# Kernel optimization log

Hardware: AMD Instinct MI355X
Metric: run time of the kernel (lower is better)

## Reference

```python
import jax, jax.numpy as jnp
import numpy as np

K = 27  # num_neighs, hardcoded in module
EPS = 1e-5


def knn_idx(x, k):
    # x: (B, N, 3) -> (B, N, k) indices of k nearest neighbors (self included)
    xx = jnp.sum(x * x, axis=-1)                      # (B, N)
    inner = jnp.einsum('bnd,bmd->bnm', x, x)          # (B, N, N)
    d = 2.0 * inner - xx[:, :, None] - xx[:, None, :] # negative sq dist
    return jax.lax.top_k(d, k)[1]


def graph_feature(f, idx):
    # f: (B, N, C), idx: (B, N, k) -> (B, N, k, 2C) = [neigh - center, center]
    neigh = jax.vmap(lambda fb, ib: fb[ib])(f, idx)   # (B, N, k, C)
    center = jnp.broadcast_to(f[:, :, None, :], neigh.shape)
    return jnp.concatenate([neigh - center, center], axis=-1)


def bn_lrelu(y, g, b, axes):
    m = jnp.mean(y, axis=axes, keepdims=True)
    v = jnp.var(y, axis=axes, keepdims=True)
    y = (y - m) * jax.lax.rsqrt(v + EPS) * g + b
    return jnp.where(y >= 0, y, 0.2 * y)


def edge_conv(f, idx, W, g, b):
    # f: (B, N, C) -> (B, N, C_out); 1x1 conv over (B, 2C, N, k) + BN + LeakyReLU + max over k
    h = graph_feature(f, idx)                         # (B, N, k, 2C)
    y = jnp.einsum('bnkc,oc->bnko', h, W)             # (B, N, k, C_out)
    y = bn_lrelu(y, g, b, axes=(0, 1, 2))
    return jnp.max(y, axis=2)                         # (B, N, C_out)


def setup_inputs() -> dict:
    key = jax.random.key(0)
    ks = jax.random.split(key, 8)
    B, N, latent = 2, 2048, 256
    x = jax.random.normal(ks[0], (B, N, 3), dtype=jnp.float32)
    chans = [(6, 96), (192, 192), (384, 384), (768, 768)]
    inp = {'x': x}
    for i, (cin, cout) in enumerate(chans):
        inp[f'W{i}'] = jax.random.normal(ks[1 + i], (cout, cin), dtype=jnp.float32) * np.sqrt(2.0 / cin).astype(np.float32)
        inp[f'g{i}'] = jnp.ones((cout,), dtype=jnp.float32)
        inp[f'b{i}'] = jnp.zeros((cout,), dtype=jnp.float32)
    inp['W4'] = jax.random.normal(ks[5], (latent, 1440), dtype=jnp.float32) * np.sqrt(2.0 / 1440).astype(np.float32)
    inp['g4'] = jnp.ones((latent,), dtype=jnp.float32)
    inp['b4'] = jnp.zeros((latent,), dtype=jnp.float32)
    return inp


def reference(x, W0, g0, b0, W1, g1, b1, W2, g2, b2, W3, g3, b3, W4, g4, b4):
    # x: (B, N, 3)
    idx = knn_idx(x, K)                               # (B, N, K), fixed for all layers (only_true_neighs=True)
    outs = []
    f = x
    for (W, g, b) in ((W0, g0, b0), (W1, g1, b1), (W2, g2, b2), (W3, g3, b3)):
        f = edge_conv(f, idx, W, g, b)
        outs.append(f)
    h = jnp.concatenate(outs, axis=-1)                # (B, N, 1440)
    y = jnp.einsum('bnc,oc->bno', h, W4)              # (B, N, latent)
    feats = bn_lrelu(y, g4, b4, axes=(0, 1))          # features_per_point (B, N, latent)
    global_feat = jnp.max(feats, axis=1)              # (B, latent)
    return global_feat, feats
```

## Files before the change

kernel.cpp:

```cpp
#include <hip/hip_runtime.h>
#include <hip/hip_bf16.h>

#define BATCH 2
#define NPB   2048
#define NPTS  4096
#define KNB   27
#define FCATC 1440
#define CSTRIDE 1696
#define NSLOT 32
#define PBATCH 4

typedef __hip_bfloat16 bf16;
typedef __attribute__((ext_vector_type(8))) short short8;
typedef __attribute__((ext_vector_type(4))) float f32x4;

__device__ __forceinline__ float b2f(bf16 v) { return __bfloat162float(v); }

__device__ __forceinline__ void split_bf16(float v, bf16& h, bf16& l) {
    h = __float2bfloat16(v);
    l = __float2bfloat16(v - b2f(h));
}

__device__ __forceinline__ float ldin(const void* p, size_t i, int f32) {
    return f32 ? ((const float*)p)[i] : b2f(((const bf16*)p)[i]);
}

__global__ void k_detect(const void* __restrict__ x, int* __restrict__ flag) {
    __shared__ int s;
    if (threadIdx.x == 0) s = 0;
    __syncthreads();
    const bf16* xb = (const bf16*)x;
    int local = 0;
    for (int i = threadIdx.x; i < NPTS * 3; i += 256) {
        float v = b2f(xb[i]);
        if (!(fabsf(v) < 1e4f)) local = 1;
    }
    if (local) s = 1;
    __syncthreads();
    if (threadIdx.x == 0) flag[0] = s;
}

__global__ void k_convx(const void* __restrict__ x, const int* __restrict__ flag, float* __restrict__ xf) {
    int i = blockIdx.x * 256 + threadIdx.x;
    if (i >= NPTS * 3) return;
    xf[i] = ldin(x, i, flag[0]);
}

__global__ void k_zero(float* p, int n) {
    int i = blockIdx.x * 256 + threadIdx.x;
    if (i < n) p[i] = 0.f;
}

__global__ __launch_bounds__(256) void k_knn(const float* __restrict__ x, int* __restrict__ idx) {
    __shared__ uint hist4[4][260];
    __shared__ uint hist[256];
    __shared__ int  tix[NPB];
    __shared__ uint s_phigh;
    __shared__ int  s_rem, s_outcnt, s_tiecnt;

    int bn = blockIdx.x, b = bn >> 11, n = bn & (NPB - 1);
    int tid = threadIdx.x;
    int wv = tid >> 6;
    const float* xb = x + (size_t)b * NPB * 3;
    float cx = xb[n * 3 + 0], cy = xb[n * 3 + 1], cz = xb[n * 3 + 2];
    float cc = cx * cx + cy * cy + cz * cz;

    uint u[8];
    #pragma unroll
    for (int j = 0; j < 8; j++) {
        int m = j * 256 + tid;
        float mx = xb[m * 3 + 0], my = xb[m * 3 + 1], mz = xb[m * 3 + 2];
        float d = 2.f * (cx * mx + cy * my + cz * mz) - cc - (mx * mx + my * my + mz * mz);
        uint s = __float_as_uint(d);
        u[j] = (s & 0x80000000u) ? ~s : (s | 0x80000000u);
    }
    if (tid == 0) { s_phigh = 0; s_rem = KNB; s_outcnt = 0; s_tiecnt = 0; }

    for (int pass = 0; pass < 4; pass++) {
        int shift = 24 - pass * 8;
        hist[tid] = 0;
        for (int i = tid; i < 4 * 260; i += 256) ((uint*)hist4)[i] = 0;
        __syncthreads();
        uint phigh = s_phigh;
        #pragma unroll
        for (int j = 0; j < 8; j++) {
            bool in = (pass == 0) || ((u[j] >> (shift + 8)) == phigh);
            if (in) atomicAdd(&hist4[wv][(u[j] >> shift) & 0xFFu], 1u);
        }
        __syncthreads();
        hist[tid] = hist4[0][tid] + hist4[1][tid] + hist4[2][tid] + hist4[3][tid];
        __syncthreads();
        if (tid < 64) {
            int L = tid;
            uint c0 = hist[L * 4 + 0], c1 = hist[L * 4 + 1], c2 = hist[L * 4 + 2], c3 = hist[L * 4 + 3];
            uint s = c0 + c1 + c2 + c3;
            uint acc = s;
            #pragma unroll
            for (int off = 1; off < 64; off <<= 1) {
                uint t = __shfl_down(acc, off);
                if (L + off < 64) acc += t;
            }
            uint excl = acc - s;
            int rem = s_rem;
            if ((int)excl < rem && (int)acc >= rem) {
                uint cs[4] = { c0, c1, c2, c3 };
                uint cum = excl;
                int bsel = 0; uint hb = 0;
                #pragma unroll
                for (int q = 3; q >= 0; q--) {
                    if ((int)cum < rem && (int)(cum + cs[q]) >= rem && hb == 0u && bsel == 0) {
                        bsel = L * 4 + q; hb = cs[q]; cum += cs[q];
                    } else if (bsel == 0 && hb == 0u) {
                        cum += cs[q];
                    }
                }
                int strictlyAbove = (int)(cum - hb);
                s_rem = rem - strictlyAbove;
                s_phigh = (phigh << 8) | (uint)bsel;
            }
        }
        __syncthreads();
    }

    uint T = s_phigh;
    #pragma unroll
    for (int j = 0; j < 8; j++) {
        int m = j * 256 + tid;
        if (u[j] > T) {
            int p = atomicAdd(&s_outcnt, 1);
            idx[bn * KNB + p] = b * NPB + m;
        } else if (u[j] == T) {
            int p = atomicAdd(&s_tiecnt, 1);
            tix[p] = m;
        }
    }
    __syncthreads();
    int outcnt = s_outcnt, rem = s_rem, tiecnt = s_tiecnt;
    if (tiecnt == rem) {
        if (tid < rem) idx[bn * KNB + outcnt + tid] = b * NPB + tix[tid];
    } else if (tid == 0) {
        for (int t = 0; t < rem; t++) {
            int bi = 0;
            for (int q = 1; q < tiecnt; q++) if (tix[q] < tix[bi]) bi = q;
            idx[bn * KNB + outcnt + t] = b * NPB + tix[bi];
            tix[bi] = 0x7fffffff;
        }
    }
}

__global__ void k_l0(const float* __restrict__ xf, const void* __restrict__ W,
                     const int* __restrict__ flag, bf16* __restrict__ Ub, float* __restrict__ Vf) {
    int i = blockIdx.x * 256 + threadIdx.x;
    if (i >= NPTS * 192) return;
    int bn = i / 192, o = i % 192;
    int f32 = flag[0];
    float x0 = xf[bn * 3 + 0], x1 = xf[bn * 3 + 1], x2 = xf[bn * 3 + 2];
    if (o < 96) {
        float r = x0 * ldin(W, o * 6 + 0, f32) + x1 * ldin(W, o * 6 + 1, f32) + x2 * ldin(W, o * 6 + 2, f32);
        Ub[(size_t)bn * 96 + o] = __float2bfloat16(r);
    } else {
        int oo = o - 96;
        float w0 = ldin(W, oo * 6 + 3, f32) - ldin(W, oo * 6 + 0, f32);
        float w1 = ldin(W, oo * 6 + 4, f32) - ldin(W, oo * 6 + 1, f32);
        float w2 = ldin(W, oo * 6 + 5, f32) - ldin(W, oo * 6 + 2, f32);
        Vf[(size_t)bn * 96 + oo] = x0 * w0 + x1 * w1 + x2 * w2;
    }
}

__global__ void k_wtT(const void* __restrict__ W, const int* __restrict__ flag,
                      bf16* __restrict__ Wh, bf16* __restrict__ Wl, int Cin, int Co) {
    int o = blockIdx.x;
    int f32 = flag[0];
    for (int c = threadIdx.x; c < Cin; c += 256) {
        float w;
        if (o < Co) {
            w = ldin(W, (size_t)o * 2 * Cin + c, f32);
        } else {
            int oo = o - Co;
            w = ldin(W, (size_t)oo * 2 * Cin + Cin + c, f32) - ldin(W, (size_t)oo * 2 * Cin + c, f32);
        }
        bf16 h, l; split_bf16(w, h, l);
        Wh[(size_t)o * Cin + c] = h;
        Wl[(size_t)o * Cin + c] = l;
    }
}

__global__ void k_wtT4(const void* __restrict__ W4, const int* __restrict__ flag,
                       bf16* __restrict__ Wh, bf16* __restrict__ Wl) {
    int i = blockIdx.x * 256 + threadIdx.x;
    if (i >= 256 * FCATC) return;
    bf16 h, l; split_bf16(ldin(W4, i, flag[0]), h, l);
    Wh[i] = h; Wl[i] = l;
}

__global__ __launch_bounds__(256) void k_gemm_mfma(const bf16* __restrict__ Ah, const bf16* __restrict__ Al,
                                                   int lda, int aoff,
                                                   const bf16* __restrict__ Bh, const bf16* __restrict__ Bl,
                                                   int K, bf16* __restrict__ Cu, float* __restrict__ Cv,
                                                   int Cosplit, int ldc, int ksz, int zstride) {
    __shared__ bf16 Ash[64][40];
    __shared__ bf16 Asl[64][40];
    __shared__ bf16 Bsh[64][40];
    __shared__ bf16 Bsl[64][40];
    int tid = threadIdx.x;
    int wave = tid >> 6, lane = tid & 63;
    int wm = wave >> 1, wn = wave & 1;
    int quad = lane >> 4, l15 = lane & 15;
    int Lxy = blockIdx.y * gridDim.x + blockIdx.x;
    int stripe = Lxy & 7;
    int w = Lxy >> 3;
    int mb = stripe * 8 + (w & 7);
    int nb = w >> 3;
    int m0 = mb * 64, n0 = nb * 64;
    int kbase = blockIdx.z * ksz;
    float* Cz = Cv + (size_t)blockIdx.z * zstride;
    int lr = tid >> 2, lc = (tid & 3) * 8;

    f32x4 acc[2][2] = {};
    for (int k0 = kbase; k0 < kbase + ksz; k0 += 32) {
        size_t ao = (size_t)(m0 + lr) * lda + aoff + k0 + lc;
        size_t bo = (size_t)(n0 + lr) * K + k0 + lc;
        *(short8*)&Ash[lr][lc] = *(const short8*)&Ah[ao];
        *(short8*)&Asl[lr][lc] = *(const short8*)&Al[ao];
        *(short8*)&Bsh[lr][lc] = *(const short8*)&Bh[bo];
        *(short8*)&Bsl[lr][lc] = *(const short8*)&Bl[bo];
        __syncthreads();
        short8 ah0 = *(const short8*)&Ash[wm * 32 + l15][quad * 8];
        short8 ah1 = *(const short8*)&Ash[wm * 32 + 16 + l15][quad * 8];
        short8 al0 = *(const short8*)&Asl[wm * 32 + l15][quad * 8];
        short8 al1 = *(const short8*)&Asl[wm * 32 + 16 + l15][quad * 8];
        short8 bh0 = *(const short8*)&Bsh[wn * 32 + l15][quad * 8];
        short8 bh1 = *(const short8*)&Bsh[wn * 32 + 16 + l15][quad * 8];
        short8 bl0 = *(const short8*)&Bsl[wn * 32 + l15][quad * 8];
        short8 bl1 = *(const short8*)&Bsl[wn * 32 + 16 + l15][quad * 8];
        acc[0][0] = __builtin_amdgcn_mfma_f32_16x16x32_bf16(ah0, bl0, acc[0][0], 0, 0, 0);
        acc[0][0] = __builtin_amdgcn_mfma_f32_16x16x32_bf16(al0, bh0, acc[0][0], 0, 0, 0);
        acc[0][0] = __builtin_amdgcn_mfma_f32_16x16x32_bf16(ah0, bh0, acc[0][0], 0, 0, 0);
        acc[0][1] = __builtin_amdgcn_mfma_f32_16x16x32_bf16(ah0, bl1, acc[0][1], 0, 0, 0);
        acc[0][1] = __builtin_amdgcn_mfma_f32_16x16x32_bf16(al0, bh1, acc[0][1], 0, 0, 0);
        acc[0][1] = __builtin_amdgcn_mfma_f32_16x16x32_bf16(ah0, bh1, acc[0][1], 0, 0, 0);
        acc[1][0] = __builtin_amdgcn_mfma_f32_16x16x32_bf16(ah1, bl0, acc[1][0], 0, 0, 0);
        acc[1][0] = __builtin_amdgcn_mfma_f32_16x16x32_bf16(al1, bh0, acc[1][0], 0, 0, 0);
        acc[1][0] = __builtin_amdgcn_mfma_f32_16x16x32_bf16(ah1, bh0, acc[1][0], 0, 0, 0);
        acc[1][1] = __builtin_amdgcn_mfma_f32_16x16x32_bf16(ah1, bl1, acc[1][1], 0, 0, 0);
        acc[1][1] = __builtin_amdgcn_mfma_f32_16x16x32_bf16(al1, bh1, acc[1][1], 0, 0, 0);
        acc[1][1] = __builtin_amdgcn_mfma_f32_16x16x32_bf16(ah1, bh1, acc[1][1], 0, 0, 0);
        __syncthreads();
    }
    #pragma unroll
    for (int mt = 0; mt < 2; mt++) {
        #pragma unroll
        for (int nt = 0; nt < 2; nt++) {
            int col = n0 + wn * 32 + nt * 16 + l15;
            #pragma unroll
            for (int i = 0; i < 4; i++) {
                int row = m0 + wm * 32 + mt * 16 + quad * 4 + i;
                if (Cosplit > 0) {
                    if (col < Cosplit) Cu[(size_t)row * Cosplit + col] = __float2bfloat16(acc[mt][nt][i]);
                    else               Cv[(size_t)row * Cosplit + col - Cosplit] = acc[mt][nt][i];
                } else {
                    Cz[(size_t)row * ldc + col] = acc[mt][nt][i];
                }
            }
        }
    }
}

__global__ __launch_bounds__(256) void k_gather(const bf16* __restrict__ Ub, float* __restrict__ Vf,
                                                const int* __restrict__ idx,
                                                bf16* __restrict__ fch, bf16* __restrict__ fcl,
                                                float* __restrict__ ssum, float* __restrict__ ssq,
                                                int Co, int out_off) {
    __shared__ int srow[PBATCH * KNB];
    int tid = threadIdx.x;
    int L = blockIdx.y * gridDim.x + blockIdx.x;
    int batch = L & 1;
    int w = L >> 1;
    int pg = batch * 512 + (w & 511);
    int chunk = w >> 9;
    int p0 = pg * PBATCH;
    if (tid < PBATCH * KNB) srow[tid] = idx[p0 * KNB + tid] * Co;
    __syncthreads();
    int o = chunk * 256 + tid;
    if (o >= Co) return;
    int slot = pg & (NSLOT - 1);
    float s = 0.f, q = 0.f;
    #pragma unroll 1
    for (int p = 0; p < PBATCH; p++) {
        int bn = p0 + p;
        float v = Vf[(size_t)bn * Co + o];
        float ymax = -INFINITY, ymin = INFINITY;
        #pragma unroll
        for (int k = 0; k < KNB; k++) {
            float y = b2f(Ub[(size_t)srow[p * KNB + k] + o]) + v;
            ymax = fmaxf(ymax, y);
            ymin = fminf(ymin, y);
            s += y; q += y * y;
        }
        bf16 h, l; split_bf16(ymax, h, l);
        fch[(size_t)bn * FCATC + out_off + o] = h;
        fcl[(size_t)bn * FCATC + out_off + o] = l;
        Vf[(size_t)bn * Co + o] = ymin;
    }
    atomicAdd(&ssum[slot * CSTRIDE + o], s);
    atomicAdd(&ssq [slot * CSTRIDE + o], q);
}

__global__ void k_scaleshift(const float* __restrict__ ssum, const float* __restrict__ ssq,
                             const void* __restrict__ g, const void* __restrict__ bb,
                             const int* __restrict__ flag,
                             float* __restrict__ scale, float* __restrict__ shift, int Co, float invcnt) {
    int o = blockIdx.x * 256 + threadIdx.x;
    if (o >= Co) return;
    int f32 = flag[0];
    float s = 0.f, q = 0.f;
    for (int c = 0; c < NSLOT; c++) { s += ssum[c * CSTRIDE + o]; q += ssq[c * CSTRIDE + o]; }
    float mean = s * invcnt;
    float var = q * invcnt - mean * mean;
    float sc = ldin(g, o, f32) * rsqrtf(var + 1e-5f);
    scale[o] = sc;
    shift[o] = ldin(bb, o, f32) - mean * sc;
}

__global__ __launch_bounds__(256) void k_apply(const float* __restrict__ Vf,
                                               const float* __restrict__ scale, const float* __restrict__ shift,
                                               bf16* __restrict__ fch, bf16* __restrict__ fcl,
                                               int Co, int out_off) {
    int bn = blockIdx.x;
    for (int o = threadIdx.x; o < Co; o += 256) {
        float sc = scale[o], sh = shift[o];
        size_t fi = (size_t)bn * FCATC + out_off + o;
        float y = (sc >= 0.f) ? (b2f(fch[fi]) + b2f(fcl[fi]))
                              : Vf[(size_t)bn * Co + o];
        float z = sc * y + sh;
        z = (z >= 0.f) ? z : 0.2f * z;
        bf16 h, l; split_bf16(z, h, l);
        fch[fi] = h; fcl[fi] = l;
    }
}

__global__ void k_stats_final(const float* __restrict__ part, float* __restrict__ Y,
                              float* __restrict__ ssum, float* __restrict__ ssq) {
    int o = threadIdx.x;
    int p0 = blockIdx.x * 128;
    const size_t PL = (size_t)NPTS * 256;
    float s = 0, q = 0;
    for (int p = 0; p < 128; p++) {
        size_t i = (size_t)(p0 + p) * 256 + o;
        float y = part[i] + part[i + PL] + part[i + 2 * PL] + part[i + 3 * PL] + part[i + 4 * PL];
        Y[i] = y;
        s += y; q += y * y;
    }
    ssum[blockIdx.x * CSTRIDE + o] = s;
    ssq [blockIdx.x * CSTRIDE + o] = q;
}

__global__ void k_feats(const float* __restrict__ Y, const float* __restrict__ scale, const float* __restrict__ shift,
                        void* __restrict__ out, const int* __restrict__ flag, float* __restrict__ partial) {
    int o = threadIdx.x;
    int chunk = blockIdx.x;
    int bn0 = chunk * 64;
    int f32 = flag[0];
    float sc = scale[o], sh = shift[o];
    float best = -INFINITY;
    for (int i = 0; i < 64; i++) {
        int bn = bn0 + i;
        float z = sc * Y[(size_t)bn * 256 + o] + sh;
        z = (z >= 0.f) ? z : 0.2f * z;
        size_t oi = (size_t)BATCH * 256 + (size_t)bn * 256 + o;
        if (f32) ((float*)out)[oi] = z;
        else     ((bf16*)out)[oi] = __float2bfloat16(z);
        best = fmaxf(best, z);
    }
    partial[chunk * 256 + o] = best;
}

__global__ void k_gmax(const float* __restrict__ partial, void* __restrict__ out, const int* __restrict__ flag) {
    int o = threadIdx.x;
    int b = blockIdx.x;
    float best = -INFINITY;
    for (int c = 0; c < 32; c++) best = fmaxf(best, partial[(b * 32 + c) * 256 + o]);
    if (flag[0]) ((float*)out)[b * 256 + o] = best;
    else         ((bf16*)out)[b * 256 + o] = __float2bfloat16(best);
}

extern "C" void kernel_launch(void* const* d_in, const int* in_sizes, int n_in,
                              void* d_out, int out_size, void* d_ws, size_t ws_size,
                              hipStream_t stream) {
    const void* x = d_in[0];

    char* ws = (char*)d_ws;
    int*   idx    = (int*)  (ws + 0);
    bf16*  Ub     = (bf16*) (ws + 442368);
    float* Vf     = (float*)(ws + 6733824);
    float* part   = (float*)(ws + 442368);
    bf16*  fch    = (bf16*) (ws + 25608192);
    bf16*  fcl    = (bf16*) (ws + 37404672);
    float* Y4     = (float*)(ws + 49201152);
    bf16*  Wh     = (bf16*) (ws + 53395456);
    bf16*  Wl     = (bf16*) (ws + 54575104);
    float* slots  = (float*)(ws + 55795456);
    float* ssum   = slots;
    float* ssq    = slots + NSLOT * CSTRIDE;
    float* scales = (float*)(ws + 58114048);
    float* shifts = scales + 1696;
    float* partial= (float*)(ws + 58141184);
    float* xf     = (float*)(ws + 58206720);
    int*   flag   = (int*)  (ws + 58255872);

    const int Cin[4]  = {3, 96, 192, 384};
    const int Co[4]   = {96, 192, 384, 768};
    const int ooff[4] = {0, 96, 288, 672};
    const int soff[5] = {0, 96, 288, 672, 1440};

    hipLaunchKernelGGL(k_detect, dim3(1), dim3(256), 0, stream, x, flag);
    hipLaunchKernelGGL(k_convx, dim3(48), dim3(256), 0, stream, x, flag, xf);
    hipLaunchKernelGGL(k_zero, dim3((2 * NSLOT * CSTRIDE + 255) / 256), dim3(256), 0, stream,
                       slots, 2 * NSLOT * CSTRIDE);
    hipLaunchKernelGGL(k_knn, dim3(NPTS), dim3(256), 0, stream, xf, idx);

    const float invcnt_edge = 1.f / (float)(NPTS * KNB);
    for (int L = 0; L < 4; L++) {
        const void* W  = d_in[1 + 3 * L];
        const void* g  = d_in[2 + 3 * L];
        const void* bb = d_in[3 + 3 * L];
        int N2 = 2 * Co[L];
        if (L == 0) {
            hipLaunchKernelGGL(k_l0, dim3((NPTS * 192 + 255) / 256), dim3(256), 0, stream,
                               xf, W, flag, Ub, Vf);
        } else {
            hipLaunchKernelGGL(k_wtT, dim3(N2), dim3(256), 0, stream, W, flag, Wh, Wl, Cin[L], Co[L]);
            hipLaunchKernelGGL(k_gemm_mfma, dim3(N2 / 64, NPTS / 64, 1), dim3(256), 0, stream,
                               fch, fcl, FCATC, ooff[L - 1], Wh, Wl, Cin[L],
                               Ub, Vf, Co[L], 0, Cin[L], 0);
        }
        hipLaunchKernelGGL(k_gather, dim3(NPTS / PBATCH, (Co[L] + 255) / 256), dim3(256), 0, stream,
                           Ub, Vf, idx, fch, fcl, ssum + soff[L], ssq + soff[L], Co[L], ooff[L]);
        hipLaunchKernelGGL(k_scaleshift, dim3((Co[L] + 255) / 256), dim3(256), 0, stream,
                           ssum + soff[L], ssq + soff[L], g, bb, flag,
                           scales + soff[L], shifts + soff[L], Co[L], invcnt_edge);
        hipLaunchKernelGGL(k_apply, dim3(NPTS), dim3(256), 0, stream,
                           Vf, scales + soff[L], shifts + soff[L], fch, fcl, Co[L], ooff[L]);
    }

    const void* W4 = d_in[13];
    const void* g4 = d_in[14];
    const void* b4 = d_in[15];
    hipLaunchKernelGGL(k_wtT4, dim3((256 * FCATC + 255) / 256), dim3(256), 0, stream, W4, flag, Wh, Wl);
    hipLaunchKernelGGL(k_gemm_mfma, dim3(256 / 64, NPTS / 64, 5), dim3(256), 0, stream,
                       fch, fcl, FCATC, 0, Wh, Wl, FCATC,
                       (bf16*)nullptr, part, 0, 256, 288, NPTS * 256);
    hipLaunchKernelGGL(k_stats_final, dim3(32), dim3(256), 0, stream, part, Y4, ssum + soff[4], ssq + soff[4]);
    hipLaunchKernelGGL(k_scaleshift, dim3(1), dim3(256), 0, stream,
                       ssum + soff[4], ssq + soff[4], g4, b4, flag,
                       scales + soff[4], shifts + soff[4], 256, 1.f / (float)NPTS);
    hipLaunchKernelGGL(k_feats, dim3(64), dim3(256), 0, stream, Y4, scales + soff[4], shifts + soff[4],
                       d_out, flag, partial);
    hipLaunchKernelGGL(k_gmax, dim3(BATCH), dim3(256), 0, stream, partial, d_out, flag);
}
```

Measured before the change: 375.4 us.

## Merge setup and weight-prep kernels and vectorize gather over channel pairs

Folds the input detection, float conversion and stat-slot zeroing into one init kernel. All four weight split/transposes now run in a single up-front kernel into a combined buffer instead of one launch per layer. The final scale/shift computation moves into k_feats. k_gather now handles two channels per thread using 32-bit bf16-pair loads and paired stores. The intent is fewer kernel launches and fewer, wider memory transactions in the gather, at the cost of more registers per gather thread and a larger weight workspace.

```diff
diff --git a/kernel.cpp b/kernel.cpp
--- a/kernel.cpp
+++ b/kernel.cpp
@@ -10,9 +10,16 @@
 #define NSLOT 32
 #define PBATCH 4
 
+#define WOFF_L1 0
+#define WOFF_L2 36864
+#define WOFF_L3 184320
+#define WOFF_F  774144
+#define WTOTAL  1142784
+
 typedef __hip_bfloat16 bf16;
 typedef __attribute__((ext_vector_type(8))) short short8;
 typedef __attribute__((ext_vector_type(4))) float f32x4;
+typedef __attribute__((ext_vector_type(2))) short s16x2;
 
 __device__ __forceinline__ float b2f(bf16 v) { return __bfloat162float(v); }
 
@@ -25,7 +32,12 @@
     return f32 ? ((const float*)p)[i] : b2f(((const bf16*)p)[i]);
 }
 
-__global__ void k_detect(const void* __restrict__ x, int* __restrict__ flag) {
+__global__ void k_init(const void* __restrict__ x, int* __restrict__ flag,
+                       float* __restrict__ xf, float* __restrict__ slots) {
+    if (blockIdx.x < 424) {
+        slots[blockIdx.x * 256 + threadIdx.x] = 0.f;
+        return;
+    }
     __shared__ int s;
     if (threadIdx.x == 0) s = 0;
     __syncthreads();
@@ -37,18 +49,9 @@
     }
     if (local) s = 1;
     __syncthreads();
-    if (threadIdx.x == 0) flag[0] = s;
-}
-
-__global__ void k_convx(const void* __restrict__ x, const int* __restrict__ flag, float* __restrict__ xf) {
-    int i = blockIdx.x * 256 + threadIdx.x;
-    if (i >= NPTS * 3) return;
-    xf[i] = ldin(x, i, flag[0]);
-}
-
-__global__ void k_zero(float* p, int n) {
-    int i = blockIdx.x * 256 + threadIdx.x;
-    if (i < n) p[i] = 0.f;
+    int f32 = s;
+    if (threadIdx.x == 0) flag[0] = f32;
+    for (int i = threadIdx.x; i < NPTS * 3; i += 256) xf[i] = ldin(x, i, f32);
 }
 
 __global__ __launch_bounds__(256) void k_knn(const float* __restrict__ x, int* __restrict__ idx) {
@@ -167,29 +170,36 @@
     }
 }
 
-__global__ void k_wtT(const void* __restrict__ W, const int* __restrict__ flag,
-                      bf16* __restrict__ Wh, bf16* __restrict__ Wl, int Cin, int Co) {
-    int o = blockIdx.x;
+__global__ void k_wt_all(const void* __restrict__ W1, const void* __restrict__ W2,
+                         const void* __restrict__ W3, const void* __restrict__ W4,
+                         const int* __restrict__ flag,
+                         bf16* __restrict__ Wh, bf16* __restrict__ Wl) {
+    int i = blockIdx.x * 256 + threadIdx.x;
+    if (i >= WTOTAL) return;
     int f32 = flag[0];
-    for (int c = threadIdx.x; c < Cin; c += 256) {
-        float w;
-        if (o < Co) {
-            w = ldin(W, (size_t)o * 2 * Cin + c, f32);
-        } else {
-            int oo = o - Co;
-            w = ldin(W, (size_t)oo * 2 * Cin + Cin + c, f32) - ldin(W, (size_t)oo * 2 * Cin + c, f32);
-        }
-        bf16 h, l; split_bf16(w, h, l);
-        Wh[(size_t)o * Cin + c] = h;
-        Wl[(size_t)o * Cin + c] = l;
-    }
-}
-
-__global__ void k_wtT4(const void* __restrict__ W4, const int* __restrict__ flag,
-                       bf16* __restrict__ Wh, bf16* __restrict__ Wl) {
-    int i = blockIdx.x * 256 + threadIdx.x;
-    if (i >= 256 * FCATC) return;
-    bf16 h, l; split_bf16(ldin(W4, i, flag[0]), h, l);
+    float w;
+    if (i < WOFF_L2) {
+        int row = i / 96, c = i % 96;
+        w = (row < 192) ? ldin(W1, (size_t)row * 192 + c, f32)
+                        : ldin(W1, (size_t)(row - 192) * 192 + 96 + c, f32)
+                          - ldin(W1, (size_t)(row - 192) * 192 + c, f32);
+    } else if (i < WOFF_L3) {
+        int j = i - WOFF_L2;
+        int row = j / 192, c = j % 192;
+        w = (row < 384) ? ldin(W2, (size_t)row * 384 + c, f32)
+                        : ldin(W2, (size_t)(row - 384) * 384 + 192 + c, f32)
+                          - ldin(W2, (size_t)(row - 384) * 384 + c, f32);
+    } else if (i < WOFF_F) {
+        int j = i - WOFF_L3;
+        int row = j / 384, c = j % 384;
+        w = (row < 768) ? ldin(W3, (size_t)row * 768 + c, f32)
+                        : ldin(W3, (size_t)(row - 768) * 768 + 384 + c, f32)
+                          - ldin(W3, (size_t)(row - 768) * 768 + c, f32);
+    } else {
+        int j = i - WOFF_F;
+        w = ldin(W4, j, f32);
+    }
+    bf16 h, l; split_bf16(w, h, l);
     Wh[i] = h; Wl[i] = l;
 }
 
@@ -281,29 +291,37 @@
     int p0 = pg * PBATCH;
     if (tid < PBATCH * KNB) srow[tid] = idx[p0 * KNB + tid] * Co;
     __syncthreads();
-    int o = chunk * 256 + tid;
-    if (o >= Co) return;
+    int P = Co >> 1;
+    int op = chunk * 256 + tid;
+    if (op >= P) return;
+    int o = op * 2;
     int slot = pg & (NSLOT - 1);
-    float s = 0.f, q = 0.f;
+    float s0 = 0.f, s1 = 0.f, q0 = 0.f, q1 = 0.f;
     #pragma unroll 1
     for (int p = 0; p < PBATCH; p++) {
         int bn = p0 + p;
-        float v = Vf[(size_t)bn * Co + o];
-        float ymax = -INFINITY, ymin = INFINITY;
+        float2 vv = *(const float2*)&Vf[(size_t)bn * Co + o];
+        float ymax0 = -INFINITY, ymax1 = -INFINITY, ymin0 = INFINITY, ymin1 = INFINITY;
         #pragma unroll
         for (int k = 0; k < KNB; k++) {
-            float y = b2f(Ub[(size_t)srow[p * KNB + k] + o]) + v;
-            ymax = fmaxf(ymax, y);
-            ymin = fminf(ymin, y);
-            s += y; q += y * y;
-        }
-        bf16 h, l; split_bf16(ymax, h, l);
-        fch[(size_t)bn * FCATC + out_off + o] = h;
-        fcl[(size_t)bn * FCATC + out_off + o] = l;
-        Vf[(size_t)bn * Co + o] = ymin;
-    }
-    atomicAdd(&ssum[slot * CSTRIDE + o], s);
-    atomicAdd(&ssq [slot * CSTRIDE + o], q);
+            uint wb = *(const uint*)&Ub[(size_t)srow[p * KNB + k] + o];
+            float y0 = __uint_as_float(wb << 16) + vv.x;
+            float y1 = __uint_as_float(wb & 0xffff0000u) + vv.y;
+            ymax0 = fmaxf(ymax0, y0); ymin0 = fminf(ymin0, y0); s0 += y0; q0 += y0 * y0;
+            ymax1 = fmaxf(ymax1, y1); ymin1 = fminf(ymin1, y1); s1 += y1; q1 += y1 * y1;
+        }
+        size_t fi = (size_t)bn * FCATC + out_off + o;
+        bf16 hh[2], ll[2];
+        split_bf16(ymax0, hh[0], ll[0]);
+        split_bf16(ymax1, hh[1], ll[1]);
+        *(s16x2*)&fch[fi] = *(const s16x2*)hh;
+        *(s16x2*)&fcl[fi] = *(const s16x2*)ll;
+        *(float2*)&Vf[(size_t)bn * Co + o] = make_float2(ymin0, ymin1);
+    }
+    atomicAdd(&ssum[slot * CSTRIDE + o + 0], s0);
+    atomicAdd(&ssum[slot * CSTRIDE + o + 1], s1);
+    atomicAdd(&ssq [slot * CSTRIDE + o + 0], q0);
+    atomicAdd(&ssq [slot * CSTRIDE + o + 1], q1);
 }
 
 __global__ void k_scaleshift(const float* __restrict__ ssum, const float* __restrict__ ssq,
@@ -355,13 +373,20 @@
     ssq [blockIdx.x * CSTRIDE + o] = q;
 }
 
-__global__ void k_feats(const float* __restrict__ Y, const float* __restrict__ scale, const float* __restrict__ shift,
-                        void* __restrict__ out, const int* __restrict__ flag, float* __restrict__ partial) {
+__global__ void k_feats(const float* __restrict__ Y, const float* __restrict__ ssum,
+                        const float* __restrict__ ssq, const void* __restrict__ g,
+                        const void* __restrict__ bb, const int* __restrict__ flag,
+                        void* __restrict__ out, float* __restrict__ partial) {
     int o = threadIdx.x;
     int chunk = blockIdx.x;
     int bn0 = chunk * 64;
     int f32 = flag[0];
-    float sc = scale[o], sh = shift[o];
+    float s = 0.f, q = 0.f;
+    for (int c = 0; c < NSLOT; c++) { s += ssum[c * CSTRIDE + o]; q += ssq[c * CSTRIDE + o]; }
+    float mean = s * (1.f / (float)NPTS);
+    float var = q * (1.f / (float)NPTS) - mean * mean;
+    float sc = ldin(g, o, f32) * rsqrtf(var + 1e-5f);
+    float sh = ldin(bb, o, f32) - mean * sc;
     float best = -INFINITY;
     for (int i = 0; i < 64; i++) {
         int bn = bn0 + i;
@@ -397,27 +422,27 @@
     bf16*  fch    = (bf16*) (ws + 25608192);
     bf16*  fcl    = (bf16*) (ws + 37404672);
     float* Y4     = (float*)(ws + 49201152);
-    bf16*  Wh     = (bf16*) (ws + 53395456);
-    bf16*  Wl     = (bf16*) (ws + 54575104);
-    float* slots  = (float*)(ws + 55795456);
+    bf16*  Whall  = (bf16*) (ws + 53395456);
+    bf16*  Wlall  = (bf16*) (ws + 55681024);
+    float* slots  = (float*)(ws + 57966592);
     float* ssum   = slots;
     float* ssq    = slots + NSLOT * CSTRIDE;
-    float* scales = (float*)(ws + 58114048);
-    float* shifts = scales + 1696;
-    float* partial= (float*)(ws + 58141184);
-    float* xf     = (float*)(ws + 58206720);
-    int*   flag   = (int*)  (ws + 58255872);
+    float* scales = (float*)(ws + 58400768);
+    float* shifts = (float*)(ws + 58407552);
+    float* partial= (float*)(ws + 58414336);
+    float* xf     = (float*)(ws + 58479872);
+    int*   flag   = (int*)  (ws + 58529024);
 
     const int Cin[4]  = {3, 96, 192, 384};
     const int Co[4]   = {96, 192, 384, 768};
     const int ooff[4] = {0, 96, 288, 672};
     const int soff[5] = {0, 96, 288, 672, 1440};
-
-    hipLaunchKernelGGL(k_detect, dim3(1), dim3(256), 0, stream, x, flag);
-    hipLaunchKernelGGL(k_convx, dim3(48), dim3(256), 0, stream, x, flag, xf);
-    hipLaunchKernelGGL(k_zero, dim3((2 * NSLOT * CSTRIDE + 255) / 256), dim3(256), 0, stream,
-                       slots, 2 * NSLOT * CSTRIDE);
+    const int woff[4] = {0, WOFF_L1, WOFF_L2, WOFF_L3};
+
+    hipLaunchKernelGGL(k_init, dim3(425), dim3(256), 0, stream, x, flag, xf, slots);
     hipLaunchKernelGGL(k_knn, dim3(NPTS), dim3(256), 0, stream, xf, idx);
+    hipLaunchKernelGGL(k_wt_all, dim3((WTOTAL + 255) / 256), dim3(256), 0, stream,
+                       d_in[4], d_in[7], d_in[10], d_in[13], flag, Whall, Wlall);
 
     const float invcnt_edge = 1.f / (float)(NPTS * KNB);
     for (int L = 0; L < 4; L++) {
@@ -429,12 +454,12 @@
             hipLaunchKernelGGL(k_l0, dim3((NPTS * 192 + 255) / 256), dim3(256), 0, stream,
                                xf, W, flag, Ub, Vf);
         } else {
-            hipLaunchKernelGGL(k_wtT, dim3(N2), dim3(256), 0, stream, W, flag, Wh, Wl, Cin[L], Co[L]);
             hipLaunchKernelGGL(k_gemm_mfma, dim3(N2 / 64, NPTS / 64, 1), dim3(256), 0, stream,
-                               fch, fcl, FCATC, ooff[L - 1], Wh, Wl, Cin[L],
+                               fch, fcl, FCATC, ooff[L - 1], Whall + woff[L], Wlall + woff[L], Cin[L],
                                Ub, Vf, Co[L], 0, Cin[L], 0);
         }
-        hipLaunchKernelGGL(k_gather, dim3(NPTS / PBATCH, (Co[L] + 255) / 256), dim3(256), 0, stream,
+        int nchunks = ((Co[L] / 2) + 255) / 256;
+        hipLaunchKernelGGL(k_gather, dim3(NPTS / PBATCH, nchunks), dim3(256), 0, stream,
                            Ub, Vf, idx, fch, fcl, ssum + soff[L], ssq + soff[L], Co[L], ooff[L]);
         hipLaunchKernelGGL(k_scaleshift, dim3((Co[L] + 255) / 256), dim3(256), 0, stream,
                            ssum + soff[L], ssq + soff[L], g, bb, flag,
@@ -443,18 +468,13 @@
                            Vf, scales + soff[L], shifts + soff[L], fch, fcl, Co[L], ooff[L]);
     }
 
-    const void* W4 = d_in[13];
     const void* g4 = d_in[14];
     const void* b4 = d_in[15];
-    hipLaunchKernelGGL(k_wtT4, dim3((256 * FCATC + 255) / 256), dim3(256), 0, stream, W4, flag, Wh, Wl);
     hipLaunchKernelGGL(k_gemm_mfma, dim3(256 / 64, NPTS / 64, 5), dim3(256), 0, stream,
-                       fch, fcl, FCATC, 0, Wh, Wl, FCATC,
+                       fch, fcl, FCATC, 0, Whall + WOFF_F, Wlall + WOFF_F, FCATC,
                        (bf16*)nullptr, part, 0, 256, 288, NPTS * 256);
     hipLaunchKernelGGL(k_stats_final, dim3(32), dim3(256), 0, stream, part, Y4, ssum + soff[4], ssq + soff[4]);
-    hipLaunchKernelGGL(k_scaleshift, dim3(1), dim3(256), 0, stream,
-                       ssum + soff[4], ssq + soff[4], g4, b4, flag,
-                       scales + soff[4], shifts + soff[4], 256, 1.f / (float)NPTS);
-    hipLaunchKernelGGL(k_feats, dim3(64), dim3(256), 0, stream, Y4, scales + soff[4], shifts + soff[4],
-                       d_out, flag, partial);
+    hipLaunchKernelGGL(k_feats, dim3(64), dim3(256), 0, stream, Y4, ssum + soff[4], ssq + soff[4],
+                       g4, b4, flag, d_out, partial);
     hipLaunchKernelGGL(k_gmax, dim3(BATCH), dim3(256), 0, stream, partial, d_out, flag);
 }
```

Measured after the change: 343.7 us. -8.4%, faster.
